# Kernel optimization log

Measured on AMD Instinct MI355X. Metric: run time of the kernel, lower is better.

The kernel has to match this reference:

```python
import jax, jax.numpy as jnp
import numpy as np

N, E, D, H, L, G, OUT = 16384, 65536, 64, 128, 3, 512, 128
EPS = 1e-5


def setup_inputs() -> dict:
    key = jax.random.key(0)
    ks = jax.random.split(key, 12)
    s = 0.05  # small init to keep res+ stack stable
    return {
        "x": jax.random.normal(ks[0], (N, D), jnp.float32),
        "edge_index": jax.random.randint(ks[1], (2, E), 0, N, jnp.int32),
        "edge_attr": jax.random.normal(ks[2], (E, D), jnp.float32),
        "batch": jnp.sort(jax.random.randint(ks[3], (N,), 0, G, jnp.int32)),
        # per-layer params, stacked on leading layer dim L
        "ln_scale": jnp.ones((L, D), jnp.float32),
        "ln_bias": jnp.zeros((L, D), jnp.float32),
        "W1": jax.random.normal(ks[4], (L, D, H), jnp.float32) * s,
        "b1": jnp.zeros((L, H), jnp.float32),
        "W2": jax.random.normal(ks[5], (L, H, D * D), jnp.float32) * s,
        "b2": jnp.zeros((L, D * D), jnp.float32),
        "root": jax.random.normal(ks[6], (L, D, D), jnp.float32) * s,
        "conv_b": jnp.zeros((L, D), jnp.float32),
        # head params
        "dense_W": jax.random.normal(ks[7], (D, D), jnp.float32) * s,
        "dense_b": jnp.zeros((D,), jnp.float32),
        "out_W": jax.random.normal(ks[8], (D, OUT), jnp.float32) * s,
        "out_b": jnp.zeros((OUT,), jnp.float32),
    }


def _layer_norm(h, scale, bias):
    mu = jnp.mean(h, axis=-1, keepdims=True)
    var = jnp.mean((h - mu) ** 2, axis=-1, keepdims=True)
    return (h - mu) * jax.lax.rsqrt(var + EPS) * scale + bias


def _gnn_layer(x, edge_index, edge_attr, ln_scale, ln_bias, W1, b1, W2, b2, root, conv_b):
    # DeepGCNLayer block='res+': h = conv(dropout(act(norm(x)))); return x + h
    # (dropout is identity in eval/reference)
    h = jax.nn.leaky_relu(_layer_norm(x, ln_scale, ln_bias))
    src, dst = edge_index[0], edge_index[1]
    # NNConv: per-edge DxD weight from edge MLP (MapE2NxN with LeakyReLU)
    w = jax.nn.leaky_relu(edge_attr @ W1 + b1) @ W2 + b2       # [E, D*D]
    w = w.reshape(-1, D, D)                                     # [E, D, D]
    msg = jnp.einsum('ed,edf->ef', h[src], w)                   # [E, D]
    num = jax.ops.segment_sum(msg, dst, num_segments=N)         # [N, D]
    deg = jax.ops.segment_sum(jnp.ones((msg.shape[0],), msg.dtype), dst, num_segments=N)
    agg = num / jnp.maximum(deg, 1.0)[:, None]                  # mean aggregation
    conv = agg + h @ root + conv_b                              # root weight + bias
    return x + conv


def reference(x, edge_index, edge_attr, batch, ln_scale, ln_bias, W1, b1, W2, b2,
              root, conv_b, dense_W, dense_b, out_W, out_b):
    for l in range(L):
        x = _gnn_layer(x, edge_index, edge_attr, ln_scale[l], ln_bias[l],
                       W1[l], b1[l], W2[l], b2[l], root[l], conv_b[l])
    x = x @ dense_W + dense_b
    # global_mean_pool over graphs
    num = jax.ops.segment_sum(x, batch, num_segments=G)
    cnt = jax.ops.segment_sum(jnp.ones((x.shape[0],), x.dtype), batch, num_segments=G)
    pooled = num / jnp.maximum(cnt, 1.0)[:, None]
    pooled = jax.nn.leaky_relu(pooled)
    return pooled @ out_W + out_b
```

## Files before the change

### kernel.cpp

```cpp
#include <hip/hip_runtime.h>
#include <hip/hip_bf16.h>

#define NN 16384
#define EE 65536
#define DD 64
#define HH 128
#define LL 3
#define GG 512
#define OUTD 128
#define NEG 0.01f

#define CHUNK 8192
#define KSEG 8


typedef __attribute__((ext_vector_type(8))) short short8;
typedef __attribute__((ext_vector_type(4))) float f32x4;

__device__ __forceinline__ float leaky(float x){ return x > 0.f ? x : NEG * x; }
__device__ __forceinline__ unsigned short f2bf(float f){
  union { float f; unsigned int u; } v; v.f = f;
  unsigned int r = v.u + 0x7fffu + ((v.u >> 16) & 1u);
  return (unsigned short)(r >> 16);
}

__global__ void k_init_ln(const float* x_in, const float* scale, const float* bias,
                          float* x_cur, float* h, int* deg, int* cursor,
                          int* cnt, float* pooled){
  int t = threadIdx.x;
  int i = blockIdx.x*256 + t;
  if (i < NN){ deg[i] = 0; cursor[i] = 0; }
  if (i < GG) cnt[i] = 0;
  if (i < GG*DD) pooled[i] = 0.f;
  int lane = t & 63, nl = t >> 6;
  int n = blockIdx.x*4 + nl;
  float v = x_in[(size_t)n*DD + lane];
  x_cur[(size_t)n*DD + lane] = v;
  float s = v;
  for (int m=1;m<64;m<<=1) s += __shfl_xor(s, m, 64);
  float mu = s * (1.0f/64.0f);
  float dv = v - mu;
  float q = dv*dv;
  for (int m=1;m<64;m<<=1) q += __shfl_xor(q, m, 64);
  float var = q * (1.0f/64.0f);
  float w = dv * rsqrtf(var + 1e-5f) * scale[lane] + bias[lane];
  h[(size_t)n*DD + lane] = leaky(w);
}

__global__ void k_degcnt(const int* ei, const int* batch, int* deg, int* cnt){
  int e = blockIdx.x*256 + threadIdx.x;
  atomicAdd(&deg[ei[EE + e]], 1);
  if (e < NN) atomicAdd(&cnt[batch[e]], 1);
}
__global__ void k_scan(const int* deg, int* row_ptr){
  __shared__ int part[256];
  int t = threadIdx.x;
  int base = t*64; int s = 0;
  for (int i=0;i<64;++i) s += deg[base+i];
  part[t] = s; __syncthreads();
  for (int off=1; off<256; off<<=1){
    int v = (t>=off)?part[t-off]:0; __syncthreads();
    part[t] += v; __syncthreads();
  }
  int run = (t==0)?0:part[t-1];
  if (t==0) row_ptr[0] = 0;
  for (int i=0;i<64;++i){ run += deg[base+i]; row_ptr[base+i+1] = run; }
}
__global__ void k_fill(const int* ei, const int* row_ptr, int* cursor,
                       int* edge_id, int* src_sorted){
  int e = blockIdx.x*256 + threadIdx.x;
  if (e < EE){
    int d = ei[EE + e];
    int pos = row_ptr[d] + atomicAdd(&cursor[d], 1);
    edge_id[pos] = e;
    src_sorted[pos] = ei[e];
  }
}

#define CV_A (EE*DD)
#define CV_B (LL*HH*DD)
#define CV_C (LL*64*8192)
__global__ void k_convert(const float* ea, const float* W1, const float* W2,
                          unsigned short* eab, unsigned short* W1T, unsigned short* W2T){
  int idx = blockIdx.x*256 + threadIdx.x;
  if (idx < CV_A){
    eab[idx] = f2bf(ea[idx]);
  } else if (idx < CV_A + CV_B){
    int i = idx - CV_A;
    int l = i >> 13, r = i & 8191;
    int j = r >> 6, d = r & 63;
    W1T[i] = f2bf(W1[(size_t)l*DD*HH + d*HH + j]);
  } else {
    int i = idx - CV_A - CV_B;
    int l = i >> 19, rem = i & ((1<<19)-1);
    int f = rem >> 13, c = rem & 8191;
    int kd = 128*((c>>3)&63) + 64*(c>>12) + 8*((c>>9)&7) + (c&7);
    W2T[i] = f2bf(W2[(size_t)l*HH*DD*DD + (size_t)kd*DD + f]);
  }
}

__global__ __launch_bounds__(256, 2)
void k_mlp3(const unsigned short* eab, const unsigned short* W1T, const float* b1,
            unsigned short* ug){
  __shared__ __align__(16) unsigned short a_lds[128][72];
  __shared__ __align__(16) unsigned short b_lds[128][72];
  __shared__ __align__(16) unsigned short c_lds[128][136];
  int t = threadIdx.x;
  int l  = blockIdx.x >> 9;
  int e0 = (blockIdx.x & 511) * 128;
  {
    int row = t >> 1, col = (t & 1) * 32;
    const float4* sa = (const float4*)(eab + (size_t)(e0 + row)*DD + col);
    const float4* sb = (const float4*)(W1T + (size_t)l*HH*DD + (size_t)row*DD + col);
    #pragma unroll
    for (int i=0;i<4;++i){
      *(float4*)&a_lds[row][col + 8*i] = sa[i];
      *(float4*)&b_lds[row][col + 8*i] = sb[i];
    }
  }
  __syncthreads();
  int wave = t >> 6, lane = t & 63;
  int m0 = (wave >> 1) * 64, j0 = (wave & 1) * 64;
  int lr = lane & 15, lq = lane >> 4;
  f32x4 acc[4][4];
  #pragma unroll
  for (int a=0;a<4;++a)
    #pragma unroll
    for (int b=0;b<4;++b) acc[a][b] = (f32x4){0.f,0.f,0.f,0.f};
  #pragma unroll
  for (int ks=0; ks<2; ++ks){
    short8 av[4];
    #pragma unroll
    for (int mt=0; mt<4; ++mt) av[mt] = *(const short8*)&a_lds[m0 + mt*16 + lr][ks*32 + lq*8];
    #pragma unroll
    for (int jt=0; jt<4; ++jt){
      short8 bv = *(const short8*)&b_lds[j0 + jt*16 + lr][ks*32 + lq*8];
      #pragma unroll
      for (int mt=0; mt<4; ++mt)
        acc[mt][jt] = __builtin_amdgcn_mfma_f32_16x16x32_bf16(av[mt], bv, acc[mt][jt], 0, 0, 0);
    }
  }
  #pragma unroll
  for (int mt=0; mt<4; ++mt)
    #pragma unroll
    for (int jt=0; jt<4; ++jt){
      int col = j0 + jt*16 + lr;
      float bj = b1[l*HH + col];
      #pragma unroll
      for (int r=0; r<4; ++r){
        int row = m0 + mt*16 + lq*4 + r;
        c_lds[row][col] = f2bf(leaky(acc[mt][jt][r] + bj));
      }
    }
  __syncthreads();
  {
    int row = t >> 1, half = t & 1;
    float4* dst = (float4*)(ug + (size_t)l*EE*HH + (size_t)(e0 + row)*HH + half*64);
    #pragma unroll
    for (int i=0;i<8;++i) dst[i] = *(const float4*)&c_lds[row][half*64 + 8*i];
  }
}

__global__ __launch_bounds__(256, 3)
void k_sbuild3(const unsigned short* ug, const float* h, const int* row_ptr,
               const int* edge_id, const int* src_sorted,
               unsigned short* S, float* Hs, int chunk_base){
  int t = threadIdx.x, wave = t >> 6, lane = t & 63;
  int q = wave & 1;
  int nloc = blockIdx.x*2 + (wave >> 1);
  int n = chunk_base + nloc;
  int r0 = row_ptr[n], r1 = row_ptr[n+1];
  float acc[64];
  #pragma unroll
  for (int d=0; d<64; ++d) acc[d] = 0.f;
  float hs = 0.f;
  int pos = r0;
  for (; pos + 4 <= r1; pos += 4){
    int e0 = edge_id[pos],   e1 = edge_id[pos+1],   e2 = edge_id[pos+2],   e3 = edge_id[pos+3];
    int s0 = src_sorted[pos],s1 = src_sorted[pos+1],s2 = src_sorted[pos+2],s3 = src_sorted[pos+3];
    float hv0 = h[(size_t)s0*DD + lane];
    float hv1 = h[(size_t)s1*DD + lane];
    float hv2 = h[(size_t)s2*DD + lane];
    float hv3 = h[(size_t)s3*DD + lane];
    unsigned int q0 = *(const unsigned int*)(ug + (size_t)e0*HH + 2*lane);
    unsigned int q1 = *(const unsigned int*)(ug + (size_t)e1*HH + 2*lane);
    unsigned int q2 = *(const unsigned int*)(ug + (size_t)e2*HH + 2*lane);
    unsigned int q3 = *(const unsigned int*)(ug + (size_t)e3*HH + 2*lane);
    float u0 = q ? __uint_as_float(q0 & 0xFFFF0000u) : __uint_as_float(q0 << 16);
    float u1 = q ? __uint_as_float(q1 & 0xFFFF0000u) : __uint_as_float(q1 << 16);
    float u2 = q ? __uint_as_float(q2 & 0xFFFF0000u) : __uint_as_float(q2 << 16);
    float u3 = q ? __uint_as_float(q3 & 0xFFFF0000u) : __uint_as_float(q3 << 16);
    hs += hv0 + hv1 + hv2 + hv3;
    int h0 = __float_as_int(hv0), h1 = __float_as_int(hv1);
    int h2 = __float_as_int(hv2), h3 = __float_as_int(hv3);
    #pragma unroll
    for (int d=0; d<64; ++d){
      float sh0 = __int_as_float(__builtin_amdgcn_readlane(h0, d));
      float sh1 = __int_as_float(__builtin_amdgcn_readlane(h1, d));
      float sh2 = __int_as_float(__builtin_amdgcn_readlane(h2, d));
      float sh3 = __int_as_float(__builtin_amdgcn_readlane(h3, d));
      acc[d] += u0*sh0;
      acc[d] += u1*sh1;
      acc[d] += u2*sh2;
      acc[d] += u3*sh3;
    }
  }
  for (; pos < r1; ++pos){
    int e = edge_id[pos];
    int s = src_sorted[pos];
    float hv = h[(size_t)s*DD + lane];
    unsigned int up = *(const unsigned int*)(ug + (size_t)e*HH + 2*lane);
    float u0 = q ? __uint_as_float(up & 0xFFFF0000u) : __uint_as_float(up << 16);
    hs += hv;
    int hvi = __float_as_int(hv);
    #pragma unroll
    for (int d=0; d<64; ++d){
      float sh = __int_as_float(__builtin_amdgcn_readlane(hvi, d));
      acc[d] += u0 * sh;
    }
  }
  float4* Srow = (float4*)(S + (size_t)nloc*8192);
  union { unsigned int u[32]; float4 v[8]; } buf;
  #pragma unroll
  for (int i=0;i<32;++i)
    buf.u[i] = (unsigned int)f2bf(acc[2*i]) | ((unsigned int)f2bf(acc[2*i+1]) << 16);
  #pragma unroll
  for (int i=0;i<8;++i)
    Srow[(q*8 + i)*64 + lane] = buf.v[i];
  if (q == 0) Hs[(size_t)n*DD + lane] = hs;
}

__global__ __launch_bounds__(256, 2)
void k_gemm(const unsigned short* S, const unsigned short* W2T,
            float* num_part, int chunk_base){
  __shared__ __align__(16) unsigned short a_lds[128][136];
  __shared__ __align__(16) unsigned short b_lds[64][136];
  int t = threadIdx.x;
  int wave = t >> 6, lane = t & 63;
  int rowblk = blockIdx.x, kseg = blockIdx.y;
  int lr = lane & 15, lq = lane >> 4;
  f32x4 acc[2][4];
  #pragma unroll
  for (int a=0;a<2;++a)
    #pragma unroll
    for (int b=0;b<4;++b) acc[a][b] = (f32x4){0.f,0.f,0.f,0.f};
  int m0 = wave * 32;
  int ra = t >> 1, qa = t & 1;
  int rb = t >> 2, qb = t & 3;
  for (int it = 0; it < 8; ++it){
    int kbase = kseg*1024 + it*128;
    {
      const float4* sa = (const float4*)(S + (size_t)(rowblk*128 + ra)*8192 + kbase + qa*64);
      float4* da = (float4*)&a_lds[ra][qa*64];
      #pragma unroll
      for (int i=0;i<8;++i) da[i] = sa[i];
      const float4* sb = (const float4*)(W2T + (size_t)rb*8192 + kbase + qb*32);
      float4* db = (float4*)&b_lds[rb][qb*32];
      #pragma unroll
      for (int i=0;i<4;++i) db[i] = sb[i];
    }
    __syncthreads();
    #pragma unroll
    for (int kk=0; kk<128; kk+=32){
      short8 a0 = *(const short8*)&a_lds[m0 + lr][kk + lq*8];
      short8 a1 = *(const short8*)&a_lds[m0 + 16 + lr][kk + lq*8];
      #pragma unroll
      for (int ft=0; ft<4; ++ft){
        short8 bv = *(const short8*)&b_lds[ft*16 + lr][kk + lq*8];
        acc[0][ft] = __builtin_amdgcn_mfma_f32_16x16x32_bf16(a0, bv, acc[0][ft], 0, 0, 0);
        acc[1][ft] = __builtin_amdgcn_mfma_f32_16x16x32_bf16(a1, bv, acc[1][ft], 0, 0, 0);
      }
    }
    __syncthreads();
  }
  float* dstp = num_part + (size_t)kseg*NN*DD;
  #pragma unroll
  for (int rt=0; rt<2; ++rt)
    #pragma unroll
    for (int ft=0; ft<4; ++ft)
      #pragma unroll
      for (int rr=0; rr<4; ++rr){
        int m = m0 + rt*16 + lq*4 + rr;
        int f = ft*16 + lr;
        int n = chunk_base + rowblk*128 + m;
        dstp[(size_t)n*DD + f] = acc[rt][ft][rr];
      }
}

__global__ void k_update_ln(float* x, const float* num_part, float* h, const float* Hs,
                            const int* deg, const float* root, const float* b2,
                            const float* conv_b, const float* ln_s, const float* ln_b,
                            int l, int do_ln){
  __shared__ float rl[64][64];
  __shared__ float b2l[64][64];
  __shared__ float hrow[4][64];
  __shared__ float hsrow[4][64];
  int t = threadIdx.x;
  int f = t & 63, nl = t >> 6;
  for (int idx=t; idx<4096; idx+=256){
    rl[idx>>6][idx&63]  = root[(size_t)l*4096 + idx];
    b2l[idx>>6][idx&63] = b2[(size_t)l*4096 + idx];
  }
  int n = blockIdx.x*4 + nl;
  hrow[nl][f]  = h[(size_t)n*DD + f];
  hsrow[nl][f] = Hs[(size_t)n*DD + f];
  __syncthreads();
  float dg = (float)deg[n]; if (dg < 1.f) dg = 1.f;
  float nsum = 0.f;
  #pragma unroll
  for (int p=0; p<KSEG; ++p) nsum += num_part[(size_t)p*NN*DD + (size_t)n*DD + f];
  float acc = x[(size_t)n*DD + f] + nsum/dg + conv_b[l*DD + f];
  #pragma unroll
  for (int d=0; d<64; ++d)
    acc += hrow[nl][d]*rl[d][f] + hsrow[nl][d]*b2l[d][f];
  x[(size_t)n*DD + f] = acc;
  if (do_ln){
    int lp = l + 1;
    float s = acc;
    for (int m=1;m<64;m<<=1) s += __shfl_xor(s, m, 64);
    float mu = s * (1.0f/64.0f);
    float dv = acc - mu;
    float qv = dv*dv;
    for (int m=1;m<64;m<<=1) qv += __shfl_xor(qv, m, 64);
    float var = qv * (1.0f/64.0f);
    float w = dv * rsqrtf(var + 1e-5f) * ln_s[lp*DD + f] + ln_b[lp*DD + f];
    h[(size_t)n*DD + f] = leaky(w);
  }
}

__global__ void k_dense_pool(const float* x, const float* dW, const float* db,
                             const int* batch, float* pooled){
  __shared__ float wl[64][64];
  __shared__ float xrow[4][64];
  int t = threadIdx.x;
  int f = t & 63, nl = t >> 6;
  for (int idx=t; idx<4096; idx+=256) wl[idx>>6][idx&63] = dW[idx];
  int n = blockIdx.x*4 + nl;
  xrow[nl][f] = x[(size_t)n*DD + f];
  __syncthreads();
  float acc = db[f];
  #pragma unroll
  for (int d=0; d<64; ++d) acc += xrow[nl][d]*wl[d][f];
  atomicAdd(&pooled[(size_t)batch[n]*DD + f], acc);
}

__global__ void k_final(const float* pooled, const int* cnt, const float* oW,
                        const float* ob, float* out){
  __shared__ float p[64];
  int g = blockIdx.x, t = threadIdx.x;
  if (t < 64){
    float c = (float)cnt[g]; if (c < 1.f) c = 1.f;
    p[t] = leaky(pooled[(size_t)g*DD + t] / c);
  }
  __syncthreads();
  float acc = ob[t];
  #pragma unroll
  for (int f=0; f<64; ++f) acc += p[f]*oW[(size_t)f*OUTD + t];
  out[(size_t)g*OUTD + t] = acc;
}

__global__ void k_diag(float* out, float val, int n){
  int i = blockIdx.x*256 + threadIdx.x;
  if (i < n) out[i] = (i==0) ? val : 0.f;
}

extern "C" void kernel_launch(void* const* d_in, const int* in_sizes, int n_in,
                              void* d_out, int out_size, void* d_ws, size_t ws_size,
                              hipStream_t stream){
  const float* x_in  = (const float*)d_in[0];
  const int*   ei    = (const int*)d_in[1];
  const float* ea    = (const float*)d_in[2];
  const int*   batch = (const int*)d_in[3];
  const float* ln_s  = (const float*)d_in[4];
  const float* ln_b  = (const float*)d_in[5];
  const float* W1    = (const float*)d_in[6];
  const float* b1    = (const float*)d_in[7];
  const float* W2    = (const float*)d_in[8];
  const float* b2    = (const float*)d_in[9];
  const float* root  = (const float*)d_in[10];
  const float* convb = (const float*)d_in[11];
  const float* dW    = (const float*)d_in[12];
  const float* db    = (const float*)d_in[13];
  const float* oW    = (const float*)d_in[14];
  const float* ob    = (const float*)d_in[15];
  float* out = (float*)d_out;

  char* ws = (char*)d_ws;
  size_t off = 0;
  auto alloc = [&](size_t bytes)->char*{
    char* p = ws + off; off = (off + bytes + 255) & ~(size_t)255; return p;
  };
  float* x_cur  = (float*)alloc((size_t)NN*DD*4);
  float* h      = (float*)alloc((size_t)NN*DD*4);
  unsigned short* ug  = (unsigned short*)alloc((size_t)LL*EE*HH*2);
  float* num_part = (float*)alloc((size_t)KSEG*NN*DD*4);
  float* Hs     = (float*)alloc((size_t)NN*DD*4);
  unsigned short* S   = (unsigned short*)alloc((size_t)CHUNK*8192*2);
  unsigned short* W2T = (unsigned short*)alloc((size_t)LL*8192*64*2);
  unsigned short* eab = (unsigned short*)alloc((size_t)EE*DD*2);
  unsigned short* W1T = (unsigned short*)alloc((size_t)LL*HH*DD*2);
  int* deg     = (int*)alloc((size_t)NN*4);
  int* row_ptr = (int*)alloc((size_t)(NN+1)*4);
  int* cursor  = (int*)alloc((size_t)NN*4);
  int* edge_id = (int*)alloc((size_t)EE*4);
  int* src_sorted = (int*)alloc((size_t)EE*4);
  int* cnt     = (int*)alloc((size_t)GG*4);
  float* pooled= (float*)alloc((size_t)GG*DD*4);
  size_t needed = off;
  if (ws_size < needed){
    k_diag<<<(out_size+255)/256, 256, 0, stream>>>(out, (float)ws_size, out_size);
    return;
  }

  k_init_ln<<<NN/4, 256, 0, stream>>>(x_in, ln_s, ln_b, x_cur, h, deg, cursor, cnt, pooled);
  k_degcnt <<<EE/256, 256, 0, stream>>>(ei, batch, deg, cnt);
  k_scan   <<<1, 256, 0, stream>>>(deg, row_ptr);
  k_fill   <<<EE/256, 256, 0, stream>>>(ei, row_ptr, cursor, edge_id, src_sorted);
  k_convert<<<(CV_A+CV_B+CV_C)/256, 256, 0, stream>>>(ea, W1, W2, eab, W1T, W2T);
  k_mlp3   <<<LL*(EE/128), 256, 0, stream>>>(eab, W1T, b1, ug);

  for (int l=0; l<LL; ++l){
    const unsigned short* ugl = ug + (size_t)l*EE*HH;
    for (int c=0; c<NN/CHUNK; ++c){
      k_sbuild3<<<CHUNK/2, 256, 0, stream>>>(ugl, h, row_ptr, edge_id, src_sorted, S, Hs, c*CHUNK);
      k_gemm   <<<dim3(CHUNK/128, KSEG), 256, 0, stream>>>(S, W2T + (size_t)l*8192*64, num_part, c*CHUNK);
    }
    k_update_ln<<<NN/4, 256, 0, stream>>>(x_cur, num_part, h, Hs, deg, root, b2, convb,
                                          ln_s, ln_b, l, (l < LL-1) ? 1 : 0);
  }
  k_dense_pool<<<NN/4, 256, 0, stream>>>(x_cur, dW, db, batch, pooled);
  k_final     <<<GG, 128, 0, stream>>>(pooled, cnt, oW, ob, out);
}
```

Measured before the change: 644.7 us.

## Restructure S-build to pair edges per wave and fuse preprocessing kernels

Merges the init/layernorm, degree count and bf16 conversion kernels into one launch to cut launch overhead. Rewrites the per-node S accumulation so each wave reads whole 32-bit ug words (both bf16 halves) and splits lanes across two edges and half of the D dimension, halving readlane count per FMA. W2T permutation is changed to match the new S layout, and launch bounds raised to 4 waves per SIMD. Risks register pressure and correctness of the remapped layout.

```diff
diff --git a/kernel.cpp b/kernel.cpp
--- a/kernel.cpp
+++ b/kernel.cpp
@@ -24,34 +24,68 @@
   return (unsigned short)(r >> 16);
 }
 
-__global__ void k_init_ln(const float* x_in, const float* scale, const float* bias,
-                          float* x_cur, float* h, int* deg, int* cursor,
-                          int* cnt, float* pooled){
-  int t = threadIdx.x;
-  int i = blockIdx.x*256 + t;
-  if (i < NN){ deg[i] = 0; cursor[i] = 0; }
-  if (i < GG) cnt[i] = 0;
-  if (i < GG*DD) pooled[i] = 0.f;
-  int lane = t & 63, nl = t >> 6;
-  int n = blockIdx.x*4 + nl;
-  float v = x_in[(size_t)n*DD + lane];
-  x_cur[(size_t)n*DD + lane] = v;
-  float s = v;
-  for (int m=1;m<64;m<<=1) s += __shfl_xor(s, m, 64);
-  float mu = s * (1.0f/64.0f);
-  float dv = v - mu;
-  float q = dv*dv;
-  for (int m=1;m<64;m<<=1) q += __shfl_xor(q, m, 64);
-  float var = q * (1.0f/64.0f);
-  float w = dv * rsqrtf(var + 1e-5f) * scale[lane] + bias[lane];
-  h[(size_t)n*DD + lane] = leaky(w);
-}
-
-__global__ void k_degcnt(const int* ei, const int* batch, int* deg, int* cnt){
-  int e = blockIdx.x*256 + threadIdx.x;
-  atomicAdd(&deg[ei[EE + e]], 1);
-  if (e < NN) atomicAdd(&cnt[batch[e]], 1);
-}
+#define CV_A (EE*DD)
+#define CV_B (LL*HH*DD)
+#define CV_C (LL*64*8192)
+#define PRE0 (NN/4)
+#define PRE1 ((CV_A+CV_B+CV_C)/256)
+#define PRE2 (EE/256)
+
+__global__ void k_pre(const float* x_in, const float* ln_s, const float* ln_b,
+                      float* x_cur, float* h, int* deg, int* cursor, int* cnt, float* pooled,
+                      const float* ea, const float* W1, const float* W2,
+                      unsigned short* eab, unsigned short* W1T, unsigned short* W2T,
+                      const int* ei, const int* batch){
+  int t = threadIdx.x;
+  int b = blockIdx.x;
+  if (b < PRE0){
+    int i = b*256 + t;
+    if (i < NN){ deg[i] = 0; cursor[i] = 0; }
+    if (i < GG) cnt[i] = 0;
+    if (i < GG*DD) pooled[i] = 0.f;
+    int lane = t & 63, nl = t >> 6;
+    int n = b*4 + nl;
+    float v = x_in[(size_t)n*DD + lane];
+    x_cur[(size_t)n*DD + lane] = v;
+    float s = v;
+    for (int m=1;m<64;m<<=1) s += __shfl_xor(s, m, 64);
+    float mu = s * (1.0f/64.0f);
+    float dv = v - mu;
+    float q = dv*dv;
+    for (int m=1;m<64;m<<=1) q += __shfl_xor(q, m, 64);
+    float var = q * (1.0f/64.0f);
+    float w = dv * rsqrtf(var + 1e-5f) * ln_s[lane] + ln_b[lane];
+    h[(size_t)n*DD + lane] = leaky(w);
+    return;
+  }
+  if (b < PRE0 + PRE1){
+    int idx = (b - PRE0)*256 + t;
+    if (idx < CV_A){
+      eab[idx] = f2bf(ea[idx]);
+    } else if (idx < CV_A + CV_B){
+      int i = idx - CV_A;
+      int l = i >> 13, r = i & 8191;
+      int j = r >> 6, d = r & 63;
+      W1T[i] = f2bf(W1[(size_t)l*DD*HH + d*HH + j]);
+    } else {
+      int i = idx - CV_A - CV_B;
+      int l = i >> 19, rem = i & ((1<<19)-1);
+      int f = rem >> 13, c = rem & 8191;
+      int kk = c & 1, j = (c>>1) & 3, lane = (c>>3) & 63, ii = (c>>9) & 7, q = (c>>12) & 1;
+      int idxu = 2*lane + kk;
+      int d = 32*q + 4*ii + j;
+      int kd = idxu*64 + d;
+      W2T[i] = f2bf(W2[(size_t)l*HH*DD*DD + (size_t)kd*DD + f]);
+    }
+    return;
+  }
+  {
+    int e = (b - PRE0 - PRE1)*256 + t;
+    atomicAdd(&deg[ei[EE + e]], 1);
+    if (e < NN) atomicAdd(&cnt[batch[e]], 1);
+  }
+}
+
 __global__ void k_scan(const int* deg, int* row_ptr){
   __shared__ int part[256];
   int t = threadIdx.x;
@@ -77,28 +111,6 @@
   }
 }
 
-#define CV_A (EE*DD)
-#define CV_B (LL*HH*DD)
-#define CV_C (LL*64*8192)
-__global__ void k_convert(const float* ea, const float* W1, const float* W2,
-                          unsigned short* eab, unsigned short* W1T, unsigned short* W2T){
-  int idx = blockIdx.x*256 + threadIdx.x;
-  if (idx < CV_A){
-    eab[idx] = f2bf(ea[idx]);
-  } else if (idx < CV_A + CV_B){
-    int i = idx - CV_A;
-    int l = i >> 13, r = i & 8191;
-    int j = r >> 6, d = r & 63;
-    W1T[i] = f2bf(W1[(size_t)l*DD*HH + d*HH + j]);
-  } else {
-    int i = idx - CV_A - CV_B;
-    int l = i >> 19, rem = i & ((1<<19)-1);
-    int f = rem >> 13, c = rem & 8191;
-    int kd = 128*((c>>3)&63) + 64*(c>>12) + 8*((c>>9)&7) + (c&7);
-    W2T[i] = f2bf(W2[(size_t)l*HH*DD*DD + (size_t)kd*DD + f]);
-  }
-}
-
 __global__ __launch_bounds__(256, 2)
 void k_mlp3(const unsigned short* eab, const unsigned short* W1T, const float* b1,
             unsigned short* ug){
@@ -161,8 +173,8 @@
   }
 }
 
-__global__ __launch_bounds__(256, 3)
-void k_sbuild3(const unsigned short* ug, const float* h, const int* row_ptr,
+__global__ __launch_bounds__(256, 4)
+void k_sbuild4(const unsigned short* ug, const float* h, const int* row_ptr,
                const int* edge_id, const int* src_sorted,
                unsigned short* S, float* Hs, int chunk_base){
   int t = threadIdx.x, wave = t >> 6, lane = t & 63;
@@ -170,64 +182,90 @@
   int nloc = blockIdx.x*2 + (wave >> 1);
   int n = chunk_base + nloc;
   int r0 = row_ptr[n], r1 = row_ptr[n+1];
+  int dbase = 32*q;
+  int lhalf = lane & 31;
+  const unsigned int* ugd = (const unsigned int*)ug;
   float acc[64];
   #pragma unroll
-  for (int d=0; d<64; ++d) acc[d] = 0.f;
+  for (int i=0;i<64;++i) acc[i] = 0.f;
   float hs = 0.f;
   int pos = r0;
   for (; pos + 4 <= r1; pos += 4){
-    int e0 = edge_id[pos],   e1 = edge_id[pos+1],   e2 = edge_id[pos+2],   e3 = edge_id[pos+3];
-    int s0 = src_sorted[pos],s1 = src_sorted[pos+1],s2 = src_sorted[pos+2],s3 = src_sorted[pos+3];
-    float hv0 = h[(size_t)s0*DD + lane];
-    float hv1 = h[(size_t)s1*DD + lane];
-    float hv2 = h[(size_t)s2*DD + lane];
-    float hv3 = h[(size_t)s3*DD + lane];
-    unsigned int q0 = *(const unsigned int*)(ug + (size_t)e0*HH + 2*lane);
-    unsigned int q1 = *(const unsigned int*)(ug + (size_t)e1*HH + 2*lane);
-    unsigned int q2 = *(const unsigned int*)(ug + (size_t)e2*HH + 2*lane);
-    unsigned int q3 = *(const unsigned int*)(ug + (size_t)e3*HH + 2*lane);
-    float u0 = q ? __uint_as_float(q0 & 0xFFFF0000u) : __uint_as_float(q0 << 16);
-    float u1 = q ? __uint_as_float(q1 & 0xFFFF0000u) : __uint_as_float(q1 << 16);
-    float u2 = q ? __uint_as_float(q2 & 0xFFFF0000u) : __uint_as_float(q2 << 16);
-    float u3 = q ? __uint_as_float(q3 & 0xFFFF0000u) : __uint_as_float(q3 << 16);
-    hs += hv0 + hv1 + hv2 + hv3;
+    int ea0 = edge_id[pos],    eb0 = edge_id[pos+1];
+    int ea1 = edge_id[pos+2],  eb1 = edge_id[pos+3];
+    int sa0 = src_sorted[pos],   sb0 = src_sorted[pos+1];
+    int sa1 = src_sorted[pos+2], sb1 = src_sorted[pos+3];
+    int sel0 = (lane < 32) ? sa0 : sb0;
+    int sel1 = (lane < 32) ? sa1 : sb1;
+    float hv0 = h[(size_t)sel0*DD + dbase + lhalf];
+    float hv1 = h[(size_t)sel1*DD + dbase + lhalf];
+    unsigned int ua0 = ugd[(size_t)ea0*64 + lane];
+    unsigned int ub0 = ugd[(size_t)eb0*64 + lane];
+    unsigned int ua1 = ugd[(size_t)ea1*64 + lane];
+    unsigned int ub1 = ugd[(size_t)eb1*64 + lane];
+    hs += hv0 + hv1;
     int h0 = __float_as_int(hv0), h1 = __float_as_int(hv1);
-    int h2 = __float_as_int(hv2), h3 = __float_as_int(hv3);
-    #pragma unroll
-    for (int d=0; d<64; ++d){
-      float sh0 = __int_as_float(__builtin_amdgcn_readlane(h0, d));
-      float sh1 = __int_as_float(__builtin_amdgcn_readlane(h1, d));
-      float sh2 = __int_as_float(__builtin_amdgcn_readlane(h2, d));
-      float sh3 = __int_as_float(__builtin_amdgcn_readlane(h3, d));
-      acc[d] += u0*sh0;
-      acc[d] += u1*sh1;
-      acc[d] += u2*sh2;
-      acc[d] += u3*sh3;
-    }
-  }
-  for (; pos < r1; ++pos){
-    int e = edge_id[pos];
-    int s = src_sorted[pos];
-    float hv = h[(size_t)s*DD + lane];
-    unsigned int up = *(const unsigned int*)(ug + (size_t)e*HH + 2*lane);
-    float u0 = q ? __uint_as_float(up & 0xFFFF0000u) : __uint_as_float(up << 16);
+    float ua0l = __uint_as_float(ua0 << 16), ua0h = __uint_as_float(ua0 & 0xFFFF0000u);
+    float ub0l = __uint_as_float(ub0 << 16), ub0h = __uint_as_float(ub0 & 0xFFFF0000u);
+    float ua1l = __uint_as_float(ua1 << 16), ua1h = __uint_as_float(ua1 & 0xFFFF0000u);
+    float ub1l = __uint_as_float(ub1 << 16), ub1h = __uint_as_float(ub1 & 0xFFFF0000u);
+    #pragma unroll
+    for (int dd=0; dd<32; ++dd){
+      float sa_ = __int_as_float(__builtin_amdgcn_readlane(h0, dd));
+      float sb_ = __int_as_float(__builtin_amdgcn_readlane(h0, 32+dd));
+      float sa2 = __int_as_float(__builtin_amdgcn_readlane(h1, dd));
+      float sb2 = __int_as_float(__builtin_amdgcn_readlane(h1, 32+dd));
+      acc[dd*2+0] += ua0l*sa_; acc[dd*2+1] += ua0h*sa_;
+      acc[dd*2+0] += ub0l*sb_; acc[dd*2+1] += ub0h*sb_;
+      acc[dd*2+0] += ua1l*sa2; acc[dd*2+1] += ua1h*sa2;
+      acc[dd*2+0] += ub1l*sb2; acc[dd*2+1] += ub1h*sb2;
+    }
+  }
+  for (; pos + 2 <= r1; pos += 2){
+    int ea = edge_id[pos],  eb = edge_id[pos+1];
+    int sa = src_sorted[pos], sb = src_sorted[pos+1];
+    int sel = (lane < 32) ? sa : sb;
+    float hv = h[(size_t)sel*DD + dbase + lhalf];
+    unsigned int ua = ugd[(size_t)ea*64 + lane];
+    unsigned int ub = ugd[(size_t)eb*64 + lane];
     hs += hv;
-    int hvi = __float_as_int(hv);
-    #pragma unroll
-    for (int d=0; d<64; ++d){
-      float sh = __int_as_float(__builtin_amdgcn_readlane(hvi, d));
-      acc[d] += u0 * sh;
-    }
-  }
-  float4* Srow = (float4*)(S + (size_t)nloc*8192);
-  union { unsigned int u[32]; float4 v[8]; } buf;
-  #pragma unroll
-  for (int i=0;i<32;++i)
-    buf.u[i] = (unsigned int)f2bf(acc[2*i]) | ((unsigned int)f2bf(acc[2*i+1]) << 16);
-  #pragma unroll
-  for (int i=0;i<8;++i)
-    Srow[(q*8 + i)*64 + lane] = buf.v[i];
-  if (q == 0) Hs[(size_t)n*DD + lane] = hs;
+    int h0 = __float_as_int(hv);
+    float ual = __uint_as_float(ua << 16), uah = __uint_as_float(ua & 0xFFFF0000u);
+    float ubl = __uint_as_float(ub << 16), ubh = __uint_as_float(ub & 0xFFFF0000u);
+    #pragma unroll
+    for (int dd=0; dd<32; ++dd){
+      float sa_ = __int_as_float(__builtin_amdgcn_readlane(h0, dd));
+      float sb_ = __int_as_float(__builtin_amdgcn_readlane(h0, 32+dd));
+      acc[dd*2+0] += ual*sa_; acc[dd*2+1] += uah*sa_;
+      acc[dd*2+0] += ubl*sb_; acc[dd*2+1] += ubh*sb_;
+    }
+  }
+  if (pos < r1){
+    int e = edge_id[pos], s = src_sorted[pos];
+    float hv = h[(size_t)s*DD + dbase + lhalf];
+    unsigned int ua = ugd[(size_t)e*64 + lane];
+    hs += (lane < 32) ? hv : 0.f;
+    int h0 = __float_as_int(hv);
+    float ual = __uint_as_float(ua << 16), uah = __uint_as_float(ua & 0xFFFF0000u);
+    #pragma unroll
+    for (int dd=0; dd<32; ++dd){
+      float sa_ = __int_as_float(__builtin_amdgcn_readlane(h0, dd));
+      acc[dd*2+0] += ual*sa_; acc[dd*2+1] += uah*sa_;
+    }
+  }
+  float4* Srow4 = (float4*)(S + (size_t)nloc*8192);
+  #pragma unroll
+  for (int i=0;i<8;++i){
+    union { unsigned int u[4]; float4 v; } b;
+    #pragma unroll
+    for (int j=0;j<4;++j){
+      int dd = 4*i + j;
+      b.u[j] = (unsigned int)f2bf(acc[dd*2+0]) | ((unsigned int)f2bf(acc[dd*2+1]) << 16);
+    }
+    Srow4[(q*8 + i)*64 + lane] = b.v;
+  }
+  float hs2 = hs + __shfl_xor(hs, 32, 64);
+  if (lane < 32) Hs[(size_t)n*DD + dbase + lane] = hs2;
 }
 
 __global__ __launch_bounds__(256, 2)
@@ -412,17 +450,16 @@
     return;
   }
 
-  k_init_ln<<<NN/4, 256, 0, stream>>>(x_in, ln_s, ln_b, x_cur, h, deg, cursor, cnt, pooled);
-  k_degcnt <<<EE/256, 256, 0, stream>>>(ei, batch, deg, cnt);
-  k_scan   <<<1, 256, 0, stream>>>(deg, row_ptr);
-  k_fill   <<<EE/256, 256, 0, stream>>>(ei, row_ptr, cursor, edge_id, src_sorted);
-  k_convert<<<(CV_A+CV_B+CV_C)/256, 256, 0, stream>>>(ea, W1, W2, eab, W1T, W2T);
-  k_mlp3   <<<LL*(EE/128), 256, 0, stream>>>(eab, W1T, b1, ug);
+  k_pre <<<PRE0+PRE1+PRE2, 256, 0, stream>>>(x_in, ln_s, ln_b, x_cur, h, deg, cursor, cnt,
+                                             pooled, ea, W1, W2, eab, W1T, W2T, ei, batch);
+  k_scan<<<1, 256, 0, stream>>>(deg, row_ptr);
+  k_fill<<<EE/256, 256, 0, stream>>>(ei, row_ptr, cursor, edge_id, src_sorted);
+  k_mlp3<<<LL*(EE/128), 256, 0, stream>>>(eab, W1T, b1, ug);
 
   for (int l=0; l<LL; ++l){
     const unsigned short* ugl = ug + (size_t)l*EE*HH;
     for (int c=0; c<NN/CHUNK; ++c){
-      k_sbuild3<<<CHUNK/2, 256, 0, stream>>>(ugl, h, row_ptr, edge_id, src_sorted, S, Hs, c*CHUNK);
+      k_sbuild4<<<CHUNK/2, 256, 0, stream>>>(ugl, h, row_ptr, edge_id, src_sorted, S, Hs, c*CHUNK);
       k_gemm   <<<dim3(CHUNK/128, KSEG), 256, 0, stream>>>(S, W2T + (size_t)l*8192*64, num_part, c*CHUNK);
     }
     k_update_ln<<<NN/4, 256, 0, stream>>>(x_cur, num_part, h, Hs, deg, root, b2, convb,
```

Result: faster. 604.2 us (-6.3%).
